# Kernel optimization log

Measured on AMD Instinct MI355X. Metric: run time of the kernel, lower is better.

Reference implementation:

```python
import jax, jax.numpy as jnp
import numpy as np

DIM = 1024
N_HEADS = 16
HEAD_DIM = DIM // N_HEADS
D_FF = 4096
EPS = 1e-6


def setup_inputs() -> dict:
    key = jax.random.key(0)
    ks = jax.random.split(key, 8)
    B, S = 2, 2048
    s = 0.02
    return {
        "x": jax.random.normal(ks[0], (B, S, DIM), dtype=jnp.float32),
        "mask": jnp.ones((B, 1, S, S), dtype=bool),
        "wq": jax.random.normal(ks[1], (DIM, DIM), dtype=jnp.float32) * s,
        "wk": jax.random.normal(ks[2], (DIM, DIM), dtype=jnp.float32) * s,
        "wv": jax.random.normal(ks[3], (DIM, DIM), dtype=jnp.float32) * s,
        "wo": jax.random.normal(ks[4], (DIM, DIM), dtype=jnp.float32) * s,
        "w_up": jax.random.normal(ks[5], (DIM, D_FF), dtype=jnp.float32) * s,
        "b_up": jnp.zeros((D_FF,), dtype=jnp.float32),
        "w_down": jax.random.normal(ks[6], (D_FF, DIM), dtype=jnp.float32) * s,
        "b_down": jnp.zeros((DIM,), dtype=jnp.float32),
        "ln1_a": jnp.ones((DIM,), dtype=jnp.float32),
        "ln1_b": jnp.zeros((DIM,), dtype=jnp.float32),
        "ln2_a": jnp.ones((DIM,), dtype=jnp.float32),
        "ln2_b": jnp.zeros((DIM,), dtype=jnp.float32),
    }


def _layernorm(x, alpha, bias):
    mu = jnp.mean(x, axis=-1, keepdims=True)
    # torch .std() is unbiased (ddof=1); denominator is (std + eps)
    sig = jnp.std(x, axis=-1, keepdims=True, ddof=1)
    return alpha * (x - mu) / (sig + EPS) + bias


def _attention(h, wq, wk, wv, wo):
    B, S, _ = h.shape
    q = (h @ wq).reshape(B, S, N_HEADS, HEAD_DIM).transpose(0, 2, 1, 3)
    k = (h @ wk).reshape(B, S, N_HEADS, HEAD_DIM).transpose(0, 2, 1, 3)
    v = (h @ wv).reshape(B, S, N_HEADS, HEAD_DIM).transpose(0, 2, 1, 3)
    scores = jnp.einsum("bhqd,bhkd->bhqk", q, k) / jnp.sqrt(jnp.float32(HEAD_DIM))
    # NOTE: original's masked_fill result is discarded -> mask is a no-op
    probs = jax.nn.softmax(scores, axis=-1)
    out = jnp.einsum("bhqk,bhkd->bhqd", probs, v)
    out = out.transpose(0, 2, 1, 3).reshape(B, S, DIM)
    return out @ wo


def reference(x, mask, wq, wk, wv, wo, w_up, b_up, w_down, b_down,
              ln1_a, ln1_b, ln2_a, ln2_b):
    h = _layernorm(x, ln1_a, ln1_b)
    x = x + _attention(h, wq, wk, wv, wo)
    h = _layernorm(x, ln2_a, ln2_b)
    ff = (jax.nn.relu(h @ w_up + b_up)) @ w_down + b_down
    return x + ff
```

## Files before the change

### kernel.cpp

```cpp
#include <hip/hip_runtime.h>
#include <hip/hip_bf16.h>

typedef __bf16 bf16_t;
typedef __bf16 bf16x8 __attribute__((ext_vector_type(8)));
typedef __bf16 bf16x4 __attribute__((ext_vector_type(4)));
typedef float  f32x4  __attribute__((ext_vector_type(4)));

#define DIM   1024
#define NHEAD 16
#define HD    64
#define DFF   4096
#define SEQ   2048
#define NTOK  4096

__device__ __forceinline__ void lgkm_barrier() {
  asm volatile("s_waitcnt lgkmcnt(0)\n\ts_barrier" ::: "memory");
}

struct TP {
  const float *wq, *wk, *wv, *wo, *wup, *wdown;
  bf16_t *wqkvT, *wupT, *wdownT;
};

__global__ __launch_bounds__(256)
void transpose_all(TP tp) {
  __shared__ bf16_t tile[32][33];
  const int id = blockIdx.x;
  const float* src; bf16_t* dst; int M, N, bx, by;
  if (id < 4096) {
    const int w = id >> 10, t = id & 1023;
    src = (w == 0) ? tp.wq : (w == 1) ? tp.wk : (w == 2) ? tp.wv : tp.wo;
    dst = tp.wqkvT + (long)w * DIM * DIM;
    M = DIM; N = DIM; bx = (t & 31) * 32; by = (t >> 5) * 32;
  } else if (id < 8192) {
    const int t = id - 4096;
    src = tp.wup; dst = tp.wupT; M = DIM; N = DFF;
    bx = (t & 127) * 32; by = (t >> 7) * 32;
  } else {
    const int t = id - 8192;
    src = tp.wdown; dst = tp.wdownT; M = DFF; N = DIM;
    bx = (t & 31) * 32; by = (t >> 5) * 32;
  }
  const int tt = threadIdx.x;
  const int r = tt >> 3, c4 = (tt & 7) * 4;
  f32x4 v = *(const f32x4*)&src[(long)(by + r) * N + bx + c4];
  tile[r][c4 + 0] = (bf16_t)v[0]; tile[r][c4 + 1] = (bf16_t)v[1];
  tile[r][c4 + 2] = (bf16_t)v[2]; tile[r][c4 + 3] = (bf16_t)v[3];
  __syncthreads();
  bf16x4 w4;
  w4[0] = tile[c4 + 0][r]; w4[1] = tile[c4 + 1][r];
  w4[2] = tile[c4 + 2][r]; w4[3] = tile[c4 + 3][r];
  *(bf16x4*)&dst[(long)(bx + r) * M + by + c4] = w4;
}

__global__ __launch_bounds__(256)
void layernorm_k(const float* __restrict__ x, const float* __restrict__ a,
                 const float* __restrict__ b, bf16_t* __restrict__ out) {
  const int row = blockIdx.x;
  const int t   = threadIdx.x;
  const float* xr = x + (long)row * DIM;
  f32x4 v = *(const f32x4*)&xr[t * 4];
  float s1 = v[0] + v[1] + v[2] + v[3];
  float s2 = v[0]*v[0] + v[1]*v[1] + v[2]*v[2] + v[3]*v[3];
  #pragma unroll
  for (int off = 32; off > 0; off >>= 1) {
    s1 += __shfl_down(s1, off);
    s2 += __shfl_down(s2, off);
  }
  __shared__ float r1[4], r2[4];
  if ((t & 63) == 0) { r1[t >> 6] = s1; r2[t >> 6] = s2; }
  __syncthreads();
  s1 = r1[0] + r1[1] + r1[2] + r1[3];
  s2 = r2[0] + r2[1] + r2[2] + r2[3];
  const float mu = s1 * (1.0f / DIM);
  float var = (s2 - (float)DIM * mu * mu) * (1.0f / (DIM - 1));
  var = fmaxf(var, 0.0f);
  const float inv = 1.0f / (sqrtf(var) + 1e-6f);
  f32x4 av = *(const f32x4*)&a[t * 4];
  f32x4 bv = *(const f32x4*)&b[t * 4];
  bf16x4 o;
  o[0] = (bf16_t)(av[0] * (v[0] - mu) * inv + bv[0]);
  o[1] = (bf16_t)(av[1] * (v[1] - mu) * inv + bv[1]);
  o[2] = (bf16_t)(av[2] * (v[2] - mu) * inv + bv[2]);
  o[3] = (bf16_t)(av[3] * (v[3] - mu) * inv + bv[3]);
  *(bf16x4*)&out[(long)row * DIM + t * 4] = o;
}

__global__ __launch_bounds__(256)
void reduce_wo_ln(const float* __restrict__ x, const bf16_t* __restrict__ p0,
                  const bf16_t* __restrict__ p1, const float* __restrict__ a,
                  const float* __restrict__ b, bf16_t* __restrict__ x1b,
                  bf16_t* __restrict__ h2) {
  const int row = blockIdx.x;
  const int t   = threadIdx.x;
  const long base = (long)row * DIM + t * 4;
  f32x4 v = *(const f32x4*)&x[base];
  bf16x4 pa = *(const bf16x4*)&p0[base];
  bf16x4 pb = *(const bf16x4*)&p1[base];
  bf16x4 xo;
  xo[0] = (bf16_t)(v[0] + (float)pa[0] + (float)pb[0]);
  xo[1] = (bf16_t)(v[1] + (float)pa[1] + (float)pb[1]);
  xo[2] = (bf16_t)(v[2] + (float)pa[2] + (float)pb[2]);
  xo[3] = (bf16_t)(v[3] + (float)pa[3] + (float)pb[3]);
  *(bf16x4*)&x1b[base] = xo;
  const float w0 = (float)xo[0], w1 = (float)xo[1], w2 = (float)xo[2], w3 = (float)xo[3];
  float s1 = w0 + w1 + w2 + w3;
  float s2 = w0*w0 + w1*w1 + w2*w2 + w3*w3;
  #pragma unroll
  for (int off = 32; off > 0; off >>= 1) {
    s1 += __shfl_down(s1, off);
    s2 += __shfl_down(s2, off);
  }
  __shared__ float r1[4], r2[4];
  if ((t & 63) == 0) { r1[t >> 6] = s1; r2[t >> 6] = s2; }
  __syncthreads();
  s1 = r1[0] + r1[1] + r1[2] + r1[3];
  s2 = r2[0] + r2[1] + r2[2] + r2[3];
  const float mu = s1 * (1.0f / DIM);
  float var = (s2 - (float)DIM * mu * mu) * (1.0f / (DIM - 1));
  var = fmaxf(var, 0.0f);
  const float inv = 1.0f / (sqrtf(var) + 1e-6f);
  f32x4 av = *(const f32x4*)&a[t * 4];
  f32x4 bv = *(const f32x4*)&b[t * 4];
  bf16x4 o;
  o[0] = (bf16_t)(av[0] * (w0 - mu) * inv + bv[0]);
  o[1] = (bf16_t)(av[1] * (w1 - mu) * inv + bv[1]);
  o[2] = (bf16_t)(av[2] * (w2 - mu) * inv + bv[2]);
  o[3] = (bf16_t)(av[3] * (w3 - mu) * inv + bv[3]);
  *(bf16x4*)&h2[(long)row * DIM + t * 4] = o;
}

__global__ __launch_bounds__(256)
void combine_att(const bf16_t* __restrict__ O1, const float* __restrict__ l0,
                 const float* __restrict__ l1, bf16_t* __restrict__ O0_attn) {
  const long i = ((long)blockIdx.x * 256 + threadIdx.x) * 4;
  const int n = (int)(i & (DIM - 1));
  const long t = i >> 10;
  const int h = n >> 6;
  const long lidx = ((t >> 11) * NHEAD + h) * SEQ + (t & (SEQ - 1));
  const float inv = 1.0f / (l0[lidx] + l1[lidx]);
  bf16x4 a = *(const bf16x4*)&O0_attn[i];
  bf16x4 b = *(const bf16x4*)&O1[i];
  bf16x4 o;
  o[0] = (bf16_t)(((float)a[0] + (float)b[0]) * inv);
  o[1] = (bf16_t)(((float)a[1] + (float)b[1]) * inv);
  o[2] = (bf16_t)(((float)a[2] + (float)b[2]) * inv);
  o[3] = (bf16_t)(((float)a[3] + (float)b[3]) * inv);
  *(bf16x4*)&O0_attn[i] = o;
}

__global__ __launch_bounds__(256)
void reduce_fd(const bf16_t* __restrict__ x1b, const float* __restrict__ bias,
               const bf16_t* __restrict__ p0, const bf16_t* __restrict__ p1,
               float* __restrict__ out) {
  const long i = ((long)blockIdx.x * 256 + threadIdx.x) * 4;
  const int n = (int)(i & (DIM - 1));
  bf16x4 xv = *(const bf16x4*)&x1b[i];
  f32x4 bv = *(const f32x4*)&bias[n];
  bf16x4 a = *(const bf16x4*)&p0[i];
  bf16x4 b = *(const bf16x4*)&p1[i];
  f32x4 o;
  o[0] = (float)xv[0] + bv[0] + (float)a[0] + (float)b[0];
  o[1] = (float)xv[1] + bv[1] + (float)a[1] + (float)b[1];
  o[2] = (float)xv[2] + bv[2] + (float)a[2] + (float)b[2];
  o[3] = (float)xv[3] + bv[3] + (float)a[3] + (float)b[3];
  *(f32x4*)&out[i] = o;
}

enum { EPI_QKV = 1, EPI_BIAS_RELU = 3, EPI_PART = 6 };

#define BM 128
#define BK 32

template <int EPI, int TBN>
__global__ __launch_bounds__(256)
void gemm_bt(const bf16_t* __restrict__ A, int lda,
             const bf16_t* __restrict__ BT, int ldb,
             bf16_t* __restrict__ Cb, bf16_t* __restrict__ Cb2,
             const float* __restrict__ bias,
             int M, int N, int Ks) {
  __shared__ bf16_t sA[2][BM][BK];
  __shared__ bf16_t sB[2][TBN][BK];
  const int tid  = threadIdx.x;
  int lin = blockIdx.x + gridDim.x * (blockIdx.y + gridDim.y * blockIdx.z);
  const int by_ = lin % gridDim.y; lin /= gridDim.y;
  const int bx_ = lin % gridDim.x;
  const int bz_ = lin / gridDim.x;
  const int m0   = by_ * BM;
  const int n0   = bx_ * TBN;
  const long koff = (long)bz_ * Ks;
  const int lane = tid & 63, wave = tid >> 6;
  constexpr int MI = (TBN == 128) ? 4 : 2;
  const int wm = (TBN == 128) ? (wave >> 1) * 64 : wave * 32;
  const int wn = (TBN == 128) ? (wave & 1) * 64 : 0;
  const int fm = lane & 15, fq = lane >> 4;

  const int lr = lane >> 2, lc = (lane & 3) * 8;
  const int lcs = lc ^ (((lr >> 1) & 3) << 3);
  const int fqs = (fq * 8) ^ (((fm >> 1) & 3) << 3);

  const bf16_t* gA0 = &A[(long)(m0 + wave * 32 + lr) * lda + koff + lc];
  const bf16_t* gA1 = gA0 + 16 * (long)lda;
  const int brow = (TBN == 128) ? wave * 32 : wave * 16;
  const bf16_t* gB0 = &BT[(long)(n0 + brow + lr) * ldb + koff + lc];
  const bf16_t* gB1 = gB0 + 16 * (long)ldb;

  f32x4 acc[MI][4] = {};
  bf16x8 rA0, rA1, rB0, rB1;

  rA0 = *(const bf16x8*)gA0;
  rA1 = *(const bf16x8*)gA1;
  rB0 = *(const bf16x8*)gB0;
  if constexpr (TBN == 128) rB1 = *(const bf16x8*)gB1;
  gA0 += BK; gA1 += BK; gB0 += BK; gB1 += BK;
  *(bf16x8*)&sA[0][wave * 32 + lr][lcs]      = rA0;
  *(bf16x8*)&sA[0][wave * 32 + 16 + lr][lcs] = rA1;
  *(bf16x8*)&sB[0][brow + lr][lcs]           = rB0;
  if constexpr (TBN == 128) *(bf16x8*)&sB[0][wave * 32 + 16 + lr][lcs] = rB1;
  if (BK < Ks) {
    rA0 = *(const bf16x8*)gA0;
    rA1 = *(const bf16x8*)gA1;
    rB0 = *(const bf16x8*)gB0;
    if constexpr (TBN == 128) rB1 = *(const bf16x8*)gB1;
    gA0 += BK; gA1 += BK; gB0 += BK; gB1 += BK;
  }
  __syncthreads();

  int p = 0;
  for (int k0 = 0; k0 < Ks; k0 += BK, p ^= 1) {
    if (k0 + BK < Ks) {
      *(bf16x8*)&sA[p ^ 1][wave * 32 + lr][lcs]      = rA0;
      *(bf16x8*)&sA[p ^ 1][wave * 32 + 16 + lr][lcs] = rA1;
      *(bf16x8*)&sB[p ^ 1][brow + lr][lcs]           = rB0;
      if constexpr (TBN == 128) *(bf16x8*)&sB[p ^ 1][wave * 32 + 16 + lr][lcs] = rB1;
      if (k0 + 2 * BK < Ks) {
        rA0 = *(const bf16x8*)gA0;
        rA1 = *(const bf16x8*)gA1;
        rB0 = *(const bf16x8*)gB0;
        if constexpr (TBN == 128) rB1 = *(const bf16x8*)gB1;
        gA0 += BK; gA1 += BK; gB0 += BK; gB1 += BK;
      }
    }
    bf16x8 af[MI], bfr[4];
    #pragma unroll
    for (int i = 0; i < MI; i++) af[i]  = *(const bf16x8*)&sA[p][wm + i * 16 + fm][fqs];
    #pragma unroll
    for (int j = 0; j < 4; j++)  bfr[j] = *(const bf16x8*)&sB[p][wn + j * 16 + fm][fqs];
    #pragma unroll
    for (int i = 0; i < MI; i++)
      #pragma unroll
      for (int j = 0; j < 4; j++)
        acc[i][j] = __builtin_amdgcn_mfma_f32_16x16x32_bf16(af[i], bfr[j], acc[i][j], 0, 0, 0);
    lgkm_barrier();
  }

  #pragma unroll
  for (int i = 0; i < MI; i++) {
    #pragma unroll
    for (int j = 0; j < 4; j++) {
      const int mb = m0 + wm + i * 16 + fq * 4;
      const int n  = n0 + wn + j * 16 + fm;
      #pragma unroll
      for (int r = 0; r < 4; r++) {
        const int m = mb + r;
        float vv = acc[i][j][r];
        if constexpr (EPI == EPI_QKV) {
          const int mat = n >> 10, h_ = (n >> 6) & 15, d_ = n & 63;
          const int b_ = m >> 11, s_ = m & 2047;
          if (mat == 2) {
            Cb2[((long)(b_ * NHEAD + h_) * HD + d_) * SEQ + s_] = (bf16_t)vv;
          } else {
            Cb[(long)mat * (32L * SEQ * HD) + (((long)(b_ * NHEAD + h_)) * SEQ + s_) * HD + d_] = (bf16_t)vv;
          }
        } else if constexpr (EPI == EPI_BIAS_RELU) {
          Cb[(long)m * N + n] = (bf16_t)fmaxf(vv + bias[n], 0.0f);
        } else {
          bf16_t* P = bz_ ? Cb2 : Cb;
          P[(long)m * N + n] = (bf16_t)vv;
        }
      }
    }
  }
}

#define KVT 128

__device__ __forceinline__ int swz(int grp, int slot) {
  return (grp * 64 + (slot ^ ((slot >> 3) & 7) ^ (grp & 1))) * 8;
}

__global__ __launch_bounds__(256)
void flash_attn(const bf16_t* __restrict__ q, const bf16_t* __restrict__ k,
                const bf16_t* __restrict__ vt,
                bf16_t* __restrict__ O0, bf16_t* __restrict__ O1,
                float* __restrict__ l0, float* __restrict__ l1) {
  __shared__ bf16_t sK[16 * 64 * 8];
  __shared__ bf16_t sV[16 * 64 * 8];

  const int tid  = threadIdx.x;
  const int bh   = blockIdx.x & 31, qb = blockIdx.x >> 5;
  const int b    = bh >> 4, h = bh & 15;
  const int lane = tid & 63, wave = tid >> 6;
  const int fm   = lane & 15, fq = lane >> 4;
  const int qw0  = qb * 128 + wave * 32;
  const int kvbase = blockIdx.y * (SEQ / 2);
  bf16_t* Op = blockIdx.y ? O1 : O0;
  float*  lp = blockIdx.y ? l1 : l0;

  const bf16_t* qh  = q  + (long)bh * SEQ * HD;
  const bf16_t* kh  = k  + (long)bh * SEQ * HD;
  const bf16_t* vth = vt + (long)bh * HD * SEQ;

  bf16x8 bQ[2][2];
  #pragma unroll
  for (int qt = 0; qt < 2; qt++)
    #pragma unroll
    for (int kk = 0; kk < 2; kk++) {
      bf16x8 v = *(const bf16x8*)&qh[(long)(qw0 + qt * 16 + fm) * HD + kk * 32 + fq * 8];
      #pragma unroll
      for (int e = 0; e < 8; e++) v[e] = (bf16_t)((float)v[e] * 0.18033688f);
      bQ[qt][kk] = v;
    }

  bf16x8 ones;
  #pragma unroll
  for (int e = 0; e < 8; e++) ones[e] = (bf16_t)1.0f;

  const int krow = tid >> 3;
  const int kc0  = (tid & 7) * 8;
  const int kh2  = (krow >> 2) & 1;
  const int kfmw = ((krow >> 3) << 2) | (krow & 3);
  const int kkk  = (tid >> 2) & 1;
  const int kfq3 = tid & 3;
  const int oK0  = swz(kh2 * 2 + kkk, kfq3 * 16 + kfmw);
  const bf16_t* pKs = kh + (long)(kvbase + krow) * HD + kc0;

  const int vd0  = tid >> 4;
  const int vc0  = (tid & 15) * 8;
  const int vu   = vc0 >> 5;
  const int vslot = ((vc0 >> 3) & 3) * 16 + vd0;
  int oV[4];
  #pragma unroll
  for (int p = 0; p < 4; p++) oV[p] = swz(vu * 4 + p, vslot);
  const bf16_t* pVs = vth + (long)vd0 * SEQ + kvbase + vc0;

  bf16x8 rK[4], rV[4];
  #pragma unroll
  for (int p = 0; p < 4; p++) {
    rK[p] = *(const bf16x8*)(pKs + p * 32 * HD);
    rV[p] = *(const bf16x8*)(pVs + p * 16 * SEQ);
  }
  pKs += KVT * HD; pVs += KVT;

  f32x4 oA[4] = {}, oB[4] = {};
  f32x4 oLA = {}, oLB = {};
  constexpr int NIT = (SEQ / 2) / KVT;

  for (int it = 0; it < NIT; it++) {
    __syncthreads();
    #pragma unroll
    for (int p = 0; p < 4; p++) {
      *(bf16x8*)&sK[oK0 + p * 2048] = rK[p];
      *(bf16x8*)&sV[oV[p]]          = rV[p];
    }
    if (it + 1 < NIT) {
      #pragma unroll
      for (int p = 0; p < 4; p++) {
        rK[p] = *(const bf16x8*)(pKs + p * 32 * HD);
        rV[p] = *(const bf16x8*)(pVs + p * 16 * SEQ);
      }
      pKs += KVT * HD; pVs += KVT;
    }
    __syncthreads();

    #pragma unroll
    for (int u = 0; u < 4; u++) {
      f32x4 stA[2], stB[2];
      #pragma unroll
      for (int h2 = 0; h2 < 2; h2++) {
        bf16x8 aK0 = *(const bf16x8*)&sK[swz((u * 2 + h2) * 2 + 0, lane)];
        bf16x8 aK1 = *(const bf16x8*)&sK[swz((u * 2 + h2) * 2 + 1, lane)];
        f32x4 z0 = {};
        z0 = __builtin_amdgcn_mfma_f32_16x16x32_bf16(aK0, bQ[0][0], z0, 0, 0, 0);
        stA[h2] = __builtin_amdgcn_mfma_f32_16x16x32_bf16(aK1, bQ[0][1], z0, 0, 0, 0);
        f32x4 z1 = {};
        z1 = __builtin_amdgcn_mfma_f32_16x16x32_bf16(aK0, bQ[1][0], z1, 0, 0, 0);
        stB[h2] = __builtin_amdgcn_mfma_f32_16x16x32_bf16(aK1, bQ[1][1], z1, 0, 0, 0);
      }
      bf16x8 pA, pB;
      #pragma unroll
      for (int h2 = 0; h2 < 2; h2++)
        #pragma unroll
        for (int r = 0; r < 4; r++) {
          pA[h2 * 4 + r] = (bf16_t)__builtin_amdgcn_exp2f(stA[h2][r]);
          pB[h2 * 4 + r] = (bf16_t)__builtin_amdgcn_exp2f(stB[h2][r]);
        }
      oLA = __builtin_amdgcn_mfma_f32_16x16x32_bf16(pA, ones, oLA, 0, 0, 0);
      oLB = __builtin_amdgcn_mfma_f32_16x16x32_bf16(pB, ones, oLB, 0, 0, 0);
      #pragma unroll
      for (int jd = 0; jd < 4; jd++) {
        bf16x8 bV = *(const bf16x8*)&sV[swz(u * 4 + jd, lane)];
        oA[jd] = __builtin_amdgcn_mfma_f32_16x16x32_bf16(pA, bV, oA[jd], 0, 0, 0);
        oB[jd] = __builtin_amdgcn_mfma_f32_16x16x32_bf16(pB, bV, oB[jd], 0, 0, 0);
      }
    }
  }

  if (fm == 0) {
    #pragma unroll
    for (int r = 0; r < 4; r++) {
      lp[(long)bh * SEQ + qw0 + fq * 4 + r]      = oLA[r];
      lp[(long)bh * SEQ + qw0 + 16 + fq * 4 + r] = oLB[r];
    }
  }

  #pragma unroll
  for (int r = 0; r < 4; r++) {
    const long rowA = ((long)b * SEQ + qw0 + fq * 4 + r) * DIM + h * HD;
    const long rowB = rowA + 16L * DIM;
    #pragma unroll
    for (int jd = 0; jd < 4; jd++) {
      Op[rowA + jd * 16 + fm] = (bf16_t)oA[jd][r];
      Op[rowB + jd * 16 + fm] = (bf16_t)oB[jd][r];
    }
  }
}

extern "C" void kernel_launch(void* const* d_in, const int* in_sizes, int n_in,
                              void* d_out, int out_size, void* d_ws, size_t ws_size,
                              hipStream_t stream) {
  (void)in_sizes; (void)n_in; (void)out_size; (void)ws_size;
  const float* x      = (const float*)d_in[0];
  const float* wq     = (const float*)d_in[2];
  const float* wk     = (const float*)d_in[3];
  const float* wv     = (const float*)d_in[4];
  const float* wo     = (const float*)d_in[5];
  const float* w_up   = (const float*)d_in[6];
  const float* b_up   = (const float*)d_in[7];
  const float* w_down = (const float*)d_in[8];
  const float* b_down = (const float*)d_in[9];
  const float* ln1a   = (const float*)d_in[10];
  const float* ln1b   = (const float*)d_in[11];
  const float* ln2a   = (const float*)d_in[12];
  const float* ln2b   = (const float*)d_in[13];

  char* ws = (char*)d_ws;
  const size_t MB = 1ull << 20;
  const size_t KB = 1ull << 10;
  float*  l0     = (float*)(ws);
  float*  l1     = (float*)(ws + 256 * KB);
  bf16_t* wqkvT  = (bf16_t*)(ws + 512 * KB);
  bf16_t* woT    = (bf16_t*)(ws + 512 * KB + 6 * MB);
  bf16_t* h      = (bf16_t*)(ws + 9 * MB);
  bf16_t* O0     = (bf16_t*)(ws + 9 * MB);
  bf16_t* attn   = (bf16_t*)(ws + 9 * MB);
  bf16_t* qkv    = (bf16_t*)(ws + 17 * MB);
  bf16_t* qd     = (bf16_t*)(ws + 17 * MB);
  bf16_t* kd     = (bf16_t*)(ws + 25 * MB);
  bf16_t* vtd    = (bf16_t*)(ws + 33 * MB);
  bf16_t* O1     = (bf16_t*)(ws + 41 * MB);
  bf16_t* p0_wo  = (bf16_t*)(ws + 17 * MB);
  bf16_t* p1_wo  = (bf16_t*)(ws + 25 * MB);
  bf16_t* x1b    = (bf16_t*)(ws + 41 * MB);
  bf16_t* h2     = (bf16_t*)(ws);
  bf16_t* wdownT = (bf16_t*)(ws + 49 * MB);
  bf16_t* wupT   = (bf16_t*)(ws + 57 * MB);
  bf16_t* ff1    = (bf16_t*)(ws + 9 * MB);
  bf16_t* p0_fd  = (bf16_t*)(ws);
  bf16_t* p1_fd  = (bf16_t*)(ws + 57 * MB);
  float*  outp   = (float*)d_out;

  const dim3 T(256);
  TP tp{wq, wk, wv, wo, w_up, w_down, wqkvT, wupT, wdownT};
  transpose_all<<<dim3(12288), T, 0, stream>>>(tp);

  layernorm_k<<<dim3(4096), T, 0, stream>>>(x, ln1a, ln1b, h);
  gemm_bt<EPI_QKV, 128><<<dim3(24, 32), T, 0, stream>>>(h, DIM, wqkvT, DIM, qkv, vtd,
                                                        nullptr, NTOK, 3072, DIM);
  flash_attn<<<dim3(512, 2), T, 0, stream>>>(qd, kd, vtd, O0, O1, l0, l1);
  combine_att<<<dim3(NTOK * DIM / 1024), T, 0, stream>>>(O1, l0, l1, attn);
  gemm_bt<EPI_PART, 64><<<dim3(16, 32, 2), T, 0, stream>>>(attn, DIM, woT, DIM, p0_wo, p1_wo,
                                                           nullptr, NTOK, DIM, DIM / 2);
  reduce_wo_ln<<<dim3(4096), T, 0, stream>>>(x, p0_wo, p1_wo, ln2a, ln2b, x1b, h2);
  gemm_bt<EPI_BIAS_RELU, 128><<<dim3(32, 32), T, 0, stream>>>(h2, DIM, wupT, DIM, ff1, nullptr,
                                                              b_up, NTOK, DFF, DIM);
  gemm_bt<EPI_PART, 64><<<dim3(16, 32, 2), T, 0, stream>>>(ff1, DFF, wdownT, DFF, p0_fd, p1_fd,
                                                           nullptr, NTOK, DIM, DFF / 2);
  reduce_fd<<<dim3(NTOK * DIM / 1024), T, 0, stream>>>(x1b, b_down, p0_fd, p1_fd, outp);
}
```

Measured before the change: 366.6 us.

## Load GEMM tiles directly into LDS with global_load_lds instead of register staging

Replaces the register-staged global→VGPR→LDS double-buffer pipeline in the GEMM kernel with direct global_load_lds 16-byte transfers into the next LDS buffer. The XOR swizzle moves from the LDS store address to the global read column, so each lane writes contiguously into LDS. This removes the VGPR staging and the ds_write instructions and may lower register pressure. In exchange, the barrier becomes a full __syncthreads that waits on vmcnt, so prefetch depth drops to one stage and the loads may overlap less with the MFMA work.

Result: no change. 363.7 us (-0.8%).

```diff
diff --git a/kernel.cpp b/kernel.cpp
--- a/kernel.cpp
+++ b/kernel.cpp
@@ -13,8 +13,10 @@
 #define SEQ   2048
 #define NTOK  4096
 
-__device__ __forceinline__ void lgkm_barrier() {
-  asm volatile("s_waitcnt lgkmcnt(0)\n\ts_barrier" ::: "memory");
+__device__ __forceinline__ void gl16(const bf16_t* g, bf16_t* l) {
+  __builtin_amdgcn_global_load_lds(
+      (const __attribute__((address_space(1))) void*)g,
+      (__attribute__((address_space(3))) void*)l, 16, 0, 0);
 }
 
 struct TP {
@@ -199,47 +201,29 @@
   const int lcs = lc ^ (((lr >> 1) & 3) << 3);
   const int fqs = (fq * 8) ^ (((fm >> 1) & 3) << 3);
 
-  const bf16_t* gA0 = &A[(long)(m0 + wave * 32 + lr) * lda + koff + lc];
+  const bf16_t* gA0 = &A[(long)(m0 + wave * 32 + lr) * lda + koff + lcs];
   const bf16_t* gA1 = gA0 + 16 * (long)lda;
   const int brow = (TBN == 128) ? wave * 32 : wave * 16;
-  const bf16_t* gB0 = &BT[(long)(n0 + brow + lr) * ldb + koff + lc];
+  const bf16_t* gB0 = &BT[(long)(n0 + brow + lr) * ldb + koff + lcs];
   const bf16_t* gB1 = gB0 + 16 * (long)ldb;
 
   f32x4 acc[MI][4] = {};
-  bf16x8 rA0, rA1, rB0, rB1;
-
-  rA0 = *(const bf16x8*)gA0;
-  rA1 = *(const bf16x8*)gA1;
-  rB0 = *(const bf16x8*)gB0;
-  if constexpr (TBN == 128) rB1 = *(const bf16x8*)gB1;
+
+  gl16(gA0, &sA[0][wave * 32][0]);
+  gl16(gA1, &sA[0][wave * 32 + 16][0]);
+  gl16(gB0, &sB[0][brow][0]);
+  if constexpr (TBN == 128) gl16(gB1, &sB[0][wave * 32 + 16][0]);
   gA0 += BK; gA1 += BK; gB0 += BK; gB1 += BK;
-  *(bf16x8*)&sA[0][wave * 32 + lr][lcs]      = rA0;
-  *(bf16x8*)&sA[0][wave * 32 + 16 + lr][lcs] = rA1;
-  *(bf16x8*)&sB[0][brow + lr][lcs]           = rB0;
-  if constexpr (TBN == 128) *(bf16x8*)&sB[0][wave * 32 + 16 + lr][lcs] = rB1;
-  if (BK < Ks) {
-    rA0 = *(const bf16x8*)gA0;
-    rA1 = *(const bf16x8*)gA1;
-    rB0 = *(const bf16x8*)gB0;
-    if constexpr (TBN == 128) rB1 = *(const bf16x8*)gB1;
-    gA0 += BK; gA1 += BK; gB0 += BK; gB1 += BK;
-  }
   __syncthreads();
 
   int p = 0;
   for (int k0 = 0; k0 < Ks; k0 += BK, p ^= 1) {
     if (k0 + BK < Ks) {
-      *(bf16x8*)&sA[p ^ 1][wave * 32 + lr][lcs]      = rA0;
-      *(bf16x8*)&sA[p ^ 1][wave * 32 + 16 + lr][lcs] = rA1;
-      *(bf16x8*)&sB[p ^ 1][brow + lr][lcs]           = rB0;
-      if constexpr (TBN == 128) *(bf16x8*)&sB[p ^ 1][wave * 32 + 16 + lr][lcs] = rB1;
-      if (k0 + 2 * BK < Ks) {
-        rA0 = *(const bf16x8*)gA0;
-        rA1 = *(const bf16x8*)gA1;
-        rB0 = *(const bf16x8*)gB0;
-        if constexpr (TBN == 128) rB1 = *(const bf16x8*)gB1;
-        gA0 += BK; gA1 += BK; gB0 += BK; gB1 += BK;
-      }
+      gl16(gA0, &sA[p ^ 1][wave * 32][0]);
+      gl16(gA1, &sA[p ^ 1][wave * 32 + 16][0]);
+      gl16(gB0, &sB[p ^ 1][brow][0]);
+      if constexpr (TBN == 128) gl16(gB1, &sB[p ^ 1][wave * 32 + 16][0]);
+      gA0 += BK; gA1 += BK; gB0 += BK; gB1 += BK;
     }
     bf16x8 af[MI], bfr[4];
     #pragma unroll
@@ -251,7 +235,7 @@
       #pragma unroll
       for (int j = 0; j < 4; j++)
         acc[i][j] = __builtin_amdgcn_mfma_f32_16x16x32_bf16(af[i], bfr[j], acc[i][j], 0, 0, 0);
-    lgkm_barrier();
+    __syncthreads();
   }
 
   #pragma unroll
```
